# Performance work log

Hardware: AMD Instinct MI355X
Metric: run time of the kernel (lower is better)

Reference implementation:

```python
import jax, jax.numpy as jnp
import numpy as np

N = 50000
E = 800000
D = 128
H = 8
DH = D // H


def setup_inputs() -> dict:
    key = jax.random.key(0)
    ks = jax.random.split(key, 8)
    x = jax.random.normal(ks[0], (N, D), dtype=jnp.float32)
    src = jax.random.randint(ks[1], (E,), 0, N, dtype=jnp.int32)
    dst = jax.random.randint(ks[2], (E,), 0, N, dtype=jnp.int32)
    s = 1.0 / np.sqrt(D)
    w_qkv = jax.random.uniform(ks[3], (3 * D, D), jnp.float32, -s, s)
    b_qkv = jax.random.uniform(ks[4], (3 * D,), jnp.float32, -s, s)
    w_out = jax.random.uniform(ks[5], (D, D), jnp.float32, -s, s)
    b_out = jax.random.uniform(ks[6], (D,), jnp.float32, -s, s)
    return {"x": x, "src": src, "dst": dst, "w_qkv": w_qkv, "b_qkv": b_qkv,
            "w_out": w_out, "b_out": b_out}


def reference(x, src, dst, w_qkv, b_qkv, w_out, b_out):
    n = x.shape[0]
    coef = 1.0 / np.sqrt(DH)
    qkv = (x @ w_qkv.T + b_qkv).reshape(n, H, 3 * DH)
    q, k, v = qkv[..., :DH], qkv[..., DH:2 * DH], qkv[..., 2 * DH:]
    # per-edge scores: dot(k[src], q[dst]) per head -> [E, H]
    scores = jnp.einsum('ehd,ehd->eh', k[src], q[dst]) * coef
    # edge softmax over edges sharing the same destination node
    smax = jax.ops.segment_max(scores, dst, num_segments=n)  # [N, H]
    smax = jnp.where(jnp.isfinite(smax), smax, 0.0)
    ex = jnp.exp(scores - smax[dst])                          # [E, H]
    denom = jax.ops.segment_sum(ex, dst, num_segments=n)      # [N, H]
    probs = ex / jnp.maximum(denom[dst], 1e-30)
    # weighted aggregation of source values -> [N, H, DH]
    agg = jax.ops.segment_sum(probs[:, :, None] * v[src], dst, num_segments=n)
    out = agg.reshape(n, D) @ w_out.T + b_out
    return out
```

## Files before the change

### kernel.cpp

```cpp
#include <hip/hip_runtime.h>
#include <math.h>

#define DD   128
#define NQKV 384
#define CAP  128

typedef __attribute__((ext_vector_type(8))) short          bf16x8;
typedef __attribute__((ext_vector_type(8))) unsigned short ushort8;
typedef __attribute__((ext_vector_type(4))) float          f32x4;
typedef __attribute__((ext_vector_type(2))) float          f32x2;

__device__ __forceinline__ unsigned short f2bf(float f) {
    unsigned u = __float_as_uint(f);
    u += 0x7fffu + ((u >> 16) & 1u);
    return (unsigned short)(u >> 16);
}
__device__ __forceinline__ float bflo(unsigned u) { return __uint_as_float(u << 16); }
__device__ __forceinline__ float bfhi(unsigned u) { return __uint_as_float(u & 0xffff0000u); }

__device__ __forceinline__ unsigned char f2e4m3(float f) {
    float a = f * 0x1p-120f;
    unsigned u = __float_as_uint(a);
    unsigned s = (u >> 24) & 0x80u;
    u &= 0x7fffffffu;
    u += 0x7ffffu + ((u >> 20) & 1u);
    unsigned mag = u >> 20;
    if (mag > 0x7eu) mag = 0x7eu;
    return (unsigned char)(s | mag);
}
__device__ __forceinline__ float e4m3f(unsigned w, int k) {
    unsigned t = w << (24 - 8 * k);
    return __uint_as_float((t & 0x80000000u) | ((t & 0x7f000000u) >> 4));
}

#if defined(__has_builtin) && __has_builtin(__builtin_amdgcn_cvt_pk_f32_fp8)
#define HW_FP8 1
#define DEC4(w, dlo, dhi)                                                   \
    f32x2 dlo = __builtin_amdgcn_cvt_pk_f32_fp8((w), 0);                    \
    f32x2 dhi = __builtin_amdgcn_cvt_pk_f32_fp8((w), 1);
#define QSCALE 1.0f
#else
#define HW_FP8 0
#define DEC4(w, dlo, dhi)                                                   \
    f32x2 dlo, dhi;                                                         \
    dlo.x = e4m3f((w), 0); dlo.y = e4m3f((w), 1);                           \
    dhi.x = e4m3f((w), 2); dhi.y = e4m3f((w), 3);
#define QSCALE 0x1p120f
#endif

#define NWQ8 (NQKV * DD / 8)
#define NWO8 (DD * DD / 8)

__global__ void prep_kernel(const float* __restrict__ x,
                            const float* __restrict__ w_qkv, const float* __restrict__ w_out,
                            unsigned short* __restrict__ xbf,
                            unsigned short* __restrict__ wqb, unsigned short* __restrict__ wob,
                            int* __restrict__ counts, int nzc4, int nx8) {
    int i = blockIdx.x * blockDim.x + threadIdx.x;
    if (i < nzc4) {
        ((int4*)counts)[i] = make_int4(0, 0, 0, 0);
        return;
    }
    int j = i - nzc4;
    const float* s;
    unsigned short* d;
    if (j < NWQ8)              { s = w_qkv + (size_t)j * 8; d = wqb + (size_t)j * 8; }
    else if (j < NWQ8 + NWO8)  { int k = j - NWQ8; s = w_out + (size_t)k * 8; d = wob + (size_t)k * 8; }
    else {
        int k = j - NWQ8 - NWO8;
        if (k >= nx8) return;
        s = x + (size_t)k * 8; d = xbf + (size_t)k * 8;
    }
    const float4* p = (const float4*)s;
    float4 a = p[0], b = p[1];
    float v[8] = {a.x, a.y, a.z, a.w, b.x, b.y, b.z, b.w};
    ushort8 vh;
    #pragma unroll
    for (int t = 0; t < 8; ++t) vh[t] = f2bf(v[t]);
    *(ushort8*)d = vh;
}

#define TM 128
#define TN 128
#define GY_QKV 170
#define GX_OUT 196

__global__ __launch_bounds__(256, 2) void scatter_qkv_kernel(
    const int* __restrict__ src, const int* __restrict__ dst,
    int* __restrict__ counts, unsigned short* __restrict__ lists, int E, int nsb,
    const unsigned short* __restrict__ Xb,
    const unsigned short* __restrict__ B,
    const float* __restrict__ bias, unsigned short* __restrict__ Cq,
    unsigned char* __restrict__ Ck8, unsigned short* __restrict__ Cv,
    int M, int mtiles)
{
    __shared__ unsigned short Bs[TN * DD];

    const int grp = (int)blockIdx.x >> 4;
    const int rr_ = (int)blockIdx.x & 15;
    if (rr_ < 7) {
        const int sblk = grp * 7 + rr_;
        if (sblk >= nsb) return;
        int t = sblk * 256 + (int)threadIdx.x;
        int base = t * 8;
        if (base >= E) return;
        if (base + 8 <= E) {
            int4 d0 = *(const int4*)(dst + base);
            int4 d1 = *(const int4*)(dst + base + 4);
            int4 s0 = *(const int4*)(src + base);
            int4 s1 = *(const int4*)(src + base + 4);
            int dd[8] = {d0.x, d0.y, d0.z, d0.w, d1.x, d1.y, d1.z, d1.w};
            int ss[8] = {s0.x, s0.y, s0.z, s0.w, s1.x, s1.y, s1.z, s1.w};
            int pos[8];
            #pragma unroll
            for (int i = 0; i < 8; ++i) pos[i] = atomicAdd(&counts[dd[i]], 1);
            #pragma unroll
            for (int i = 0; i < 8; ++i)
                if (pos[i] < CAP) lists[(size_t)dd[i] * CAP + pos[i]] = (unsigned short)ss[i];
        } else {
            for (int e = base; e < E; ++e) {
                int d = dst[e];
                int pos = atomicAdd(&counts[d], 1);
                if (pos < CAP) lists[(size_t)d * CAP + pos] = (unsigned short)src[e];
            }
        }
        return;
    }

    const int qb = grp * 9 + (rr_ - 7);
    if (qb >= 3 * GY_QKV) return;
    const int tid  = threadIdx.x;
    const int l    = tid & 63;
    const int wv   = tid >> 6;
    const int quad = l >> 4;
    const int l15  = l & 15;
    const int wm   = (wv & 1) * 64;
    const int wn   = (wv >> 1) * 64;
    const int n0   = (qb % 3) * TN;
    const int mt_start = qb / 3;

    const size_t gbase = (size_t)n0 * DD;
    for (int i = tid; i < TN * 16; i += 256) {
        int col = i >> 4, g = i & 15;
        int gs  = g ^ (col & 15);
        *(ushort8*)&Bs[col * DD + gs * 8] = *(const ushort8*)(B + gbase + (size_t)col * DD + g * 8);
    }
    __syncthreads();

    for (int mt0 = mt_start; mt0 < mtiles; mt0 += GY_QKV) {
        const int m0 = mt0 * TM;

        f32x4 acc[4][4];
        #pragma unroll
        for (int i = 0; i < 4; ++i)
            #pragma unroll
            for (int j = 0; j < 4; ++j) acc[i][j] = (f32x4)0.f;

        bf16x8 af[4][4];
        #pragma unroll
        for (int mt = 0; mt < 4; ++mt) {
            const unsigned short* ar = Xb + (size_t)(m0 + wm + mt * 16 + l15) * DD + quad * 8;
            #pragma unroll
            for (int kq = 0; kq < 4; ++kq) af[mt][kq] = *(const bf16x8*)(ar + kq * 32);
        }

        #pragma unroll
        for (int kq = 0; kq < 4; ++kq) {
            bf16x8 bh[4];
            #pragma unroll
            for (int nt = 0; nt < 4; ++nt) {
                int colL = wn + nt * 16 + l15;
                int gs   = (kq * 4 + quad) ^ (colL & 15);
                bh[nt] = *(const bf16x8*)&Bs[colL * DD + gs * 8];
            }
            #pragma unroll
            for (int mt = 0; mt < 4; ++mt)
                #pragma unroll
                for (int nt = 0; nt < 4; ++nt)
                    acc[mt][nt] = __builtin_amdgcn_mfma_f32_16x16x32_bf16(af[mt][kq], bh[nt], acc[mt][nt], 0, 0, 0);
        }

        #pragma unroll
        for (int nt = 0; nt < 4; ++nt) {
            int j = n0 + wn + nt * 16 + l15;
            float bj = bias[j];
            int h = j / 48;
            int r = j - h * 48;
            int seg = (r >= 32) ? 2 : ((r >= 16) ? 1 : 0);
            int bc  = h * 16 + r - seg * 16;
            if (seg == 1) {
                #pragma unroll
                for (int mt = 0; mt < 4; ++mt)
                    #pragma unroll
                    for (int rr = 0; rr < 4; ++rr) {
                        int m = m0 + wm + mt * 16 + quad * 4 + rr;
                        if (m < M) Ck8[(size_t)m * DD + bc] = f2e4m3(acc[mt][nt][rr] + bj);
                    }
            } else {
                unsigned short* dstp = (seg == 0 ? Cq : Cv);
                #pragma unroll
                for (int mt = 0; mt < 4; ++mt)
                    #pragma unroll
                    for (int rr = 0; rr < 4; ++rr) {
                        int m = m0 + wm + mt * 16 + quad * 4 + rr;
                        if (m < M) dstp[(size_t)m * DD + bc] = f2bf(acc[mt][nt][rr] + bj);
                    }
            }
        }
    }
}

__global__ __launch_bounds__(256, 2) void out_gemm_kernel(
    const unsigned short* __restrict__ A,
    const unsigned short* __restrict__ B,
    const float* __restrict__ bias, float* __restrict__ C, int M, int mtiles)
{
    __shared__ unsigned short Bs[TN * DD];

    const int tid  = threadIdx.x;
    const int l    = tid & 63;
    const int wv   = tid >> 6;
    const int quad = l >> 4;
    const int l15  = l & 15;
    const int wm   = (wv & 1) * 64;
    const int wn   = (wv >> 1) * 64;

    for (int i = tid; i < TN * 16; i += 256) {
        int col = i >> 4, g = i & 15;
        int gs  = g ^ (col & 15);
        *(ushort8*)&Bs[col * DD + gs * 8] = *(const ushort8*)(B + (size_t)col * DD + g * 8);
    }
    __syncthreads();

    for (int mt0 = blockIdx.x; mt0 < mtiles; mt0 += gridDim.x) {
        const int m0 = mt0 * TM;

        f32x4 acc[4][4];
        #pragma unroll
        for (int i = 0; i < 4; ++i)
            #pragma unroll
            for (int j = 0; j < 4; ++j) acc[i][j] = (f32x4)0.f;

        bf16x8 af[4][4];
        #pragma unroll
        for (int mt = 0; mt < 4; ++mt) {
            const int mrow = m0 + wm + mt * 16 + l15;
            const int mclamp = (mrow < M) ? mrow : (M - 1);
            #pragma unroll
            for (int kq = 0; kq < 4; ++kq)
                af[mt][kq] = *(const bf16x8*)(A + (size_t)mclamp * DD + kq * 32 + quad * 8);
        }

        #pragma unroll
        for (int kq = 0; kq < 4; ++kq) {
            bf16x8 bh[4];
            #pragma unroll
            for (int nt = 0; nt < 4; ++nt) {
                int colL = wn + nt * 16 + l15;
                int gs   = (kq * 4 + quad) ^ (colL & 15);
                bh[nt] = *(const bf16x8*)&Bs[colL * DD + gs * 8];
            }
            #pragma unroll
            for (int mt = 0; mt < 4; ++mt)
                #pragma unroll
                for (int nt = 0; nt < 4; ++nt)
                    acc[mt][nt] = __builtin_amdgcn_mfma_f32_16x16x32_bf16(af[mt][kq], bh[nt], acc[mt][nt], 0, 0, 0);
        }

        #pragma unroll
        for (int nt = 0; nt < 4; ++nt) {
            int j = wn + nt * 16 + l15;
            float bj = bias[j];
            #pragma unroll
            for (int mt = 0; mt < 4; ++mt)
                #pragma unroll
                for (int rr = 0; rr < 4; ++rr) {
                    int m = m0 + wm + mt * 16 + quad * 4 + rr;
                    if (m < M) C[(size_t)m * DD + j] = acc[mt][nt][rr] + bj;
                }
        }
    }
}

#define ATTN_BLOCKS 2048

#define ATTN_STEP(cka, cvv, nka, nvv)                                             \
  {                                                                                \
    const int cnt  = min(8, deg - c);                                              \
    const bool more = (c + 8 < deg);                                               \
    const int nn = (int)lists[row0 + min(c + 16 + e, deg - 1)];                    \
    if (more) {                                                                    \
      nka = *(const uint4*)(kb8 + ((((unsigned)nxt) << 7) + hoff));                \
      _Pragma("unroll")                                                            \
      for (int ee = 0; ee < 8; ++ee)                                               \
        nvv[ee] = *(const unsigned*)(vb8 + ((((unsigned)__shfl(nxt, ee)) << 8) + loff4)); \
    }                                                                              \
                        \
    DEC4(cka.x, dax, day)                                                          \
    float sA = dax.x * q0.x;                                                       \
    sA = fmaf(dax.y, q0.y, sA);                                                    \
    sA = fmaf(day.x, q0.z, sA);                                                    \
    sA = fmaf(day.y, q0.w, sA);                                                    \
    DEC4(cka.y, dbx, dby)                                                          \
    float sB = dbx.x * q1.x;                                                       \
    sB = fmaf(dbx.y, q1.y, sB);                                                    \
    sB = fmaf(dby.x, q1.z, sB);                                                    \
    sB = fmaf(dby.y, q1.w, sB);                                                    \
    DEC4(cka.z, dcx, dcy)                                                          \
    float sC = dcx.x * q2.x;                                                       \
    sC = fmaf(dcx.y, q2.y, sC);                                                    \
    sC = fmaf(dcy.x, q2.z, sC);                                                    \
    sC = fmaf(dcy.y, q2.w, sC);                                                    \
    DEC4(cka.w, ddx, ddy)                                                          \
    float sD = ddx.x * q3.x;                                                       \
    sD = fmaf(ddx.y, q3.y, sD);                                                    \
    sD = fmaf(ddy.x, q3.z, sD);                                                    \
    sD = fmaf(ddy.y, q3.w, sD);                                                    \
    const float s_ = (sA + sB) + (sC + sD);                                        \
    const float pp = __expf(s_ * 0.25f);                           \
    const float p_ = (e < cnt) ? pp : 0.f;                                         \
    l_run += p_;                                                                   \
    _Pragma("unroll")                                                              \
    for (int ee = 0; ee < 8; ++ee) {                                               \
      const float pe = __shfl(p_, lbase | ee);          \
      if ((ee & 1) == 0) {                                                         \
        acc0a = fmaf(pe, bflo(cvv[ee]), acc0a);                                    \
        acc1a = fmaf(pe, bfhi(cvv[ee]), acc1a);                                    \
      } else {                                                                     \
        acc0b = fmaf(pe, bflo(cvv[ee]), acc0b);                                    \
        acc1b = fmaf(pe, bfhi(cvv[ee]), acc1b);                                    \
      }                                                                            \
    }                                                                              \
    nxt = nn;                                                                      \
    c += 8;                                                                        \
  }

__global__ __launch_bounds__(256) void wave_attn_kernel(
    const unsigned short* __restrict__ qbf, const unsigned char* __restrict__ k8,
    const unsigned short* __restrict__ vbf, const unsigned short* __restrict__ lists,
    const int* __restrict__ counts,
    unsigned short* __restrict__ agg, int N)
{
    const int lane   = threadIdx.x & 63;
    const int wid    = blockIdx.x * 4 + (threadIdx.x >> 6);
    const int nwaves = gridDim.x * 4;

    const int h = lane >> 3;
    const int e = lane & 7;
    const unsigned hoff  = (unsigned)h << 4;
    const unsigned loff4 = (unsigned)lane << 2;
    const int lbase = lane & 0x38;

    const char* kb8 = (const char*)k8;
    const char* vb8 = (const char*)vbf;
    const char* qb8 = (const char*)qbf;
    char*       ab8 = (char*)agg;

    for (int n = wid; n < N; n += nwaves) {
        const int deg = min(counts[n], CAP);
        const unsigned ooff = (((unsigned)n) << 8) + loff4;
        if (deg == 0) {
            *(unsigned*)(ab8 + ooff) = 0u;
            continue;
        }

        const int row0 = n * CAP;

        const unsigned qoff = (((unsigned)n) << 8) + ((unsigned)h << 5);
        const uint4 qa = *(const uint4*)(qb8 + qoff);
        const uint4 qb = *(const uint4*)(qb8 + qoff + 16);
        const float S = QSCALE;
        const float4 q0 = make_float4(bflo(qa.x)*S, bfhi(qa.x)*S, bflo(qa.y)*S, bfhi(qa.y)*S);
        const float4 q1 = make_float4(bflo(qa.z)*S, bfhi(qa.z)*S, bflo(qa.w)*S, bfhi(qa.w)*S);
        const float4 q2 = make_float4(bflo(qb.x)*S, bfhi(qb.x)*S, bflo(qb.y)*S, bfhi(qb.y)*S);
        const float4 q3 = make_float4(bflo(qb.z)*S, bfhi(qb.z)*S, bflo(qb.w)*S, bfhi(qb.w)*S);

        const int c0s = (int)lists[row0 + min(e, deg - 1)];
        int nxt       = (int)lists[row0 + min(8 + e, deg - 1)];

        uint4 ka0, ka1;
        unsigned vv0[8], vv1[8];
        {
            ka0 = *(const uint4*)(kb8 + ((((unsigned)c0s) << 7) + hoff));
            #pragma unroll
            for (int ee = 0; ee < 8; ++ee)
                vv0[ee] = *(const unsigned*)(vb8 + ((((unsigned)__shfl(c0s, ee)) << 8) + loff4));
        }
        ka1 = ka0;
        #pragma unroll
        for (int ee = 0; ee < 8; ++ee) vv1[ee] = 0u;

        float l_run = 0.f;
        float acc0a = 0.f, acc0b = 0.f, acc1a = 0.f, acc1b = 0.f;

        int c = 0;
        for (;;) {
            ATTN_STEP(ka0, vv0, ka1, vv1);
            if (c >= deg) break;
            ATTN_STEP(ka1, vv1, ka0, vv0);
            if (c >= deg) break;
        }

        l_run += __shfl_xor(l_run, 1);
        l_run += __shfl_xor(l_run, 2);
        l_run += __shfl_xor(l_run, 4);

        const float inv = 1.f / fmaxf(l_run, 1e-30f);
        const float o0 = (acc0a + acc0b) * inv, o1 = (acc1a + acc1b) * inv;
        *(unsigned*)(ab8 + ooff) = (unsigned)f2bf(o0) | ((unsigned)f2bf(o1) << 16);
    }
}

extern "C" void kernel_launch(void* const* d_in, const int* in_sizes, int n_in,
                              void* d_out, int out_size, void* d_ws, size_t ws_size,
                              hipStream_t stream) {
    const float* x     = (const float*)d_in[0];
    const int*   src   = (const int*)  d_in[1];
    const int*   dst   = (const int*)  d_in[2];
    const float* w_qkv = (const float*)d_in[3];
    const float* b_qkv = (const float*)d_in[4];
    const float* w_out = (const float*)d_in[5];
    const float* b_out = (const float*)d_in[6];
    float* out = (float*)d_out;

    const int N = in_sizes[0] / DD;
    const int E = in_sizes[1];

    typedef unsigned short u16;
    char* ws = (char*)d_ws;
    u16* qbf   = (u16*)ws;           ws += (size_t)N * DD * sizeof(u16);
    unsigned char* k8 = (unsigned char*)ws; ws += (size_t)N * DD;
    u16* vbf   = (u16*)ws;           ws += (size_t)N * DD * sizeof(u16);
    u16* aggb  = (u16*)ws;           ws += (size_t)N * DD * sizeof(u16);
    u16* wqb   = (u16*)ws;           ws += (size_t)NQKV * DD * sizeof(u16);
    u16* wob   = (u16*)ws;           ws += (size_t)DD * DD * sizeof(u16);
    int* counts = (int*)ws;          ws += (size_t)((N + 3) / 4 * 4) * sizeof(int);
    u16* lists  = (u16*)ws;          ws += (size_t)N * CAP * sizeof(u16);

    u16* xbf = aggb;

    const int nx8  = N * DD / 8;
    const int nzc4 = (N + 3) / 4;
    const int npb  = (nzc4 + NWQ8 + NWO8 + nx8 + 255) / 256;
    const int nsb  = ((E + 7) / 8 + 255) / 256;
    const int MB   = (N + TM - 1) / TM;
    const int NQB  = 3 * GY_QKV;
    const int ngrp = max((nsb + 6) / 7, (NQB + 8) / 9);

    prep_kernel<<<npb, 256, 0, stream>>>(x, w_qkv, w_out, xbf, wqb, wob,
                                         counts, nzc4, nx8);
    scatter_qkv_kernel<<<ngrp * 16, 256, 0, stream>>>(
        src, dst, counts, lists, E, nsb,
        xbf, wqb, b_qkv, qbf, k8, vbf, N, MB);

    wave_attn_kernel<<<ATTN_BLOCKS, 256, 0, stream>>>(
        qbf, k8, vbf, lists, counts, aggb, N);

    out_gemm_kernel<<<GX_OUT, 256, 0, stream>>>(
        aggb, wob, b_out, out, N, MB);
}
```

Before: 192.9 us.

## Replace fixed-capacity adjacency lists with CSR via count, prefix scan, scatter

```diff
diff --git a/kernel.cpp b/kernel.cpp
--- a/kernel.cpp
+++ b/kernel.cpp
@@ -3,7 +3,6 @@
 
 #define DD   128
 #define NQKV 384
-#define CAP  128
 
 typedef __attribute__((ext_vector_type(8))) short          bf16x8;
 typedef __attribute__((ext_vector_type(8))) unsigned short ushort8;
@@ -34,13 +33,11 @@
 }
 
 #if defined(__has_builtin) && __has_builtin(__builtin_amdgcn_cvt_pk_f32_fp8)
-#define HW_FP8 1
 #define DEC4(w, dlo, dhi)                                                   \
     f32x2 dlo = __builtin_amdgcn_cvt_pk_f32_fp8((w), 0);                    \
     f32x2 dhi = __builtin_amdgcn_cvt_pk_f32_fp8((w), 1);
 #define QSCALE 1.0f
 #else
-#define HW_FP8 0
 #define DEC4(w, dlo, dhi)                                                   \
     f32x2 dlo, dhi;                                                         \
     dlo.x = e4m3f((w), 0); dlo.y = e4m3f((w), 1);                           \
@@ -53,24 +50,32 @@
 
 __global__ void prep_kernel(const float* __restrict__ x,
                             const float* __restrict__ w_qkv, const float* __restrict__ w_out,
+                            const int* __restrict__ dst,
                             unsigned short* __restrict__ xbf,
                             unsigned short* __restrict__ wqb, unsigned short* __restrict__ wob,
-                            int* __restrict__ counts, int nzc4, int nx8) {
-    int i = blockIdx.x * blockDim.x + threadIdx.x;
-    if (i < nzc4) {
-        ((int4*)counts)[i] = make_int4(0, 0, 0, 0);
+                            int* __restrict__ counts, int nx8, int E) {
+    int j = blockIdx.x * blockDim.x + threadIdx.x;
+    if (j >= NWQ8 + NWO8 + nx8) {
+        int k = j - NWQ8 - NWO8 - nx8;
+        int base = k * 8;
+        if (base >= E) return;
+        if (base + 8 <= E) {
+            int4 d0 = *(const int4*)(dst + base);
+            int4 d1 = *(const int4*)(dst + base + 4);
+            atomicAdd(&counts[d0.x], 1); atomicAdd(&counts[d0.y], 1);
+            atomicAdd(&counts[d0.z], 1); atomicAdd(&counts[d0.w], 1);
+            atomicAdd(&counts[d1.x], 1); atomicAdd(&counts[d1.y], 1);
+            atomicAdd(&counts[d1.z], 1); atomicAdd(&counts[d1.w], 1);
+        } else {
+            for (int e = base; e < E; ++e) atomicAdd(&counts[dst[e]], 1);
+        }
         return;
     }
-    int j = i - nzc4;
     const float* s;
     unsigned short* d;
     if (j < NWQ8)              { s = w_qkv + (size_t)j * 8; d = wqb + (size_t)j * 8; }
     else if (j < NWQ8 + NWO8)  { int k = j - NWQ8; s = w_out + (size_t)k * 8; d = wob + (size_t)k * 8; }
-    else {
-        int k = j - NWQ8 - NWO8;
-        if (k >= nx8) return;
-        s = x + (size_t)k * 8; d = xbf + (size_t)k * 8;
-    }
+    else                       { int k = j - NWQ8 - NWO8; s = x + (size_t)k * 8; d = xbf + (size_t)k * 8; }
     const float4* p = (const float4*)s;
     float4 a = p[0], b = p[1];
     float v[8] = {a.x, a.y, a.z, a.w, b.x, b.y, b.z, b.w};
@@ -80,6 +85,38 @@
     *(ushort8*)d = vh;
 }
 
+#define SCAN_PER 49
+__global__ __launch_bounds__(1024) void prefix_kernel(const int* __restrict__ counts,
+                                                      int* __restrict__ offsets,
+                                                      int* __restrict__ cursors, int N) {
+    __shared__ int sc[1024];
+    const int t = threadIdx.x;
+    const int base = t * SCAN_PER;
+    int s = 0;
+    for (int i = 0; i < SCAN_PER; ++i) {
+        int n = base + i;
+        if (n < N) s += counts[n];
+    }
+    sc[t] = s;
+    __syncthreads();
+    for (int d = 1; d < 1024; d <<= 1) {
+        int v = (t >= d) ? sc[t - d] : 0;
+        __syncthreads();
+        sc[t] += v;
+        __syncthreads();
+    }
+    int off = (t == 0) ? 0 : sc[t - 1];
+    for (int i = 0; i < SCAN_PER; ++i) {
+        int n = base + i;
+        if (n < N) {
+            offsets[n] = off;
+            cursors[n] = off;
+            off += counts[n];
+        }
+    }
+    if (t == 1023) offsets[N] = sc[1023];
+}
+
 #define TM 128
 #define TN 128
 #define GY_QKV 170
@@ -87,7 +124,7 @@
 
 __global__ __launch_bounds__(256, 2) void scatter_qkv_kernel(
     const int* __restrict__ src, const int* __restrict__ dst,
-    int* __restrict__ counts, unsigned short* __restrict__ lists, int E, int nsb,
+    int* __restrict__ cursors, unsigned short* __restrict__ lists, int E, int nsb,
     const unsigned short* __restrict__ Xb,
     const unsigned short* __restrict__ B,
     const float* __restrict__ bias, unsigned short* __restrict__ Cq,
@@ -113,15 +150,13 @@
             int ss[8] = {s0.x, s0.y, s0.z, s0.w, s1.x, s1.y, s1.z, s1.w};
             int pos[8];
             #pragma unroll
-            for (int i = 0; i < 8; ++i) pos[i] = atomicAdd(&counts[dd[i]], 1);
-            #pragma unroll
-            for (int i = 0; i < 8; ++i)
-                if (pos[i] < CAP) lists[(size_t)dd[i] * CAP + pos[i]] = (unsigned short)ss[i];
+            for (int i = 0; i < 8; ++i) pos[i] = atomicAdd(&cursors[dd[i]], 1);
+            #pragma unroll
+            for (int i = 0; i < 8; ++i) lists[pos[i]] = (unsigned short)ss[i];
         } else {
             for (int e = base; e < E; ++e) {
-                int d = dst[e];
-                int pos = atomicAdd(&counts[d], 1);
-                if (pos < CAP) lists[(size_t)d * CAP + pos] = (unsigned short)src[e];
+                int pos = atomicAdd(&cursors[dst[e]], 1);
+                lists[pos] = (unsigned short)src[e];
             }
         }
         return;
@@ -338,7 +373,7 @@
 __global__ __launch_bounds__(256) void wave_attn_kernel(
     const unsigned short* __restrict__ qbf, const unsigned char* __restrict__ k8,
     const unsigned short* __restrict__ vbf, const unsigned short* __restrict__ lists,
-    const int* __restrict__ counts,
+    const int* __restrict__ offsets,
     unsigned short* __restrict__ agg, int N)
 {
     const int lane   = threadIdx.x & 63;
@@ -357,14 +392,13 @@
     char*       ab8 = (char*)agg;
 
     for (int n = wid; n < N; n += nwaves) {
-        const int deg = min(counts[n], CAP);
+        const int row0 = offsets[n];
+        const int deg  = offsets[n + 1] - row0;
         const unsigned ooff = (((unsigned)n) << 8) + loff4;
         if (deg == 0) {
             *(unsigned*)(ab8 + ooff) = 0u;
             continue;
         }
-
-        const int row0 = n * CAP;
 
         const unsigned qoff = (((unsigned)n) << 8) + ((unsigned)h << 5);
         const uint4 qa = *(const uint4*)(qb8 + qoff);
@@ -434,27 +468,31 @@
     u16* aggb  = (u16*)ws;           ws += (size_t)N * DD * sizeof(u16);
     u16* wqb   = (u16*)ws;           ws += (size_t)NQKV * DD * sizeof(u16);
     u16* wob   = (u16*)ws;           ws += (size_t)DD * DD * sizeof(u16);
-    int* counts = (int*)ws;          ws += (size_t)((N + 3) / 4 * 4) * sizeof(int);
-    u16* lists  = (u16*)ws;          ws += (size_t)N * CAP * sizeof(u16);
+    int* counts  = (int*)ws;         ws += (size_t)N * sizeof(int);
+    int* offsets = (int*)ws;         ws += (size_t)(N + 1) * sizeof(int);
+    int* cursors = (int*)ws;         ws += (size_t)N * sizeof(int);
+    u16* lists   = (u16*)ws;         ws += (size_t)((E + 3) / 4 * 4) * sizeof(u16);
 
     u16* xbf = aggb;
 
     const int nx8  = N * DD / 8;
-    const int nzc4 = (N + 3) / 4;
-    const int npb  = (nzc4 + NWQ8 + NWO8 + nx8 + 255) / 256;
-    const int nsb  = ((E + 7) / 8 + 255) / 256;
+    const int nh8  = (E + 7) / 8;
+    const int npb  = (NWQ8 + NWO8 + nx8 + nh8 + 255) / 256;
+    const int nsb  = (nh8 + 255) / 256;
     const int MB   = (N + TM - 1) / TM;
     const int NQB  = 3 * GY_QKV;
     const int ngrp = max((nsb + 6) / 7, (NQB + 8) / 9);
 
-    prep_kernel<<<npb, 256, 0, stream>>>(x, w_qkv, w_out, xbf, wqb, wob,
-                                         counts, nzc4, nx8);
+    hipMemsetAsync(counts, 0, (size_t)N * sizeof(int), stream);
+    prep_kernel<<<npb, 256, 0, stream>>>(x, w_qkv, w_out, dst, xbf, wqb, wob,
+                                         counts, nx8, E);
+    prefix_kernel<<<1, 1024, 0, stream>>>(counts, offsets, cursors, N);
     scatter_qkv_kernel<<<ngrp * 16, 256, 0, stream>>>(
-        src, dst, counts, lists, E, nsb,
+        src, dst, cursors, lists, E, nsb,
         xbf, wqb, b_qkv, qbf, k8, vbf, N, MB);
 
     wave_attn_kernel<<<ATTN_BLOCKS, 256, 0, stream>>>(
-        qbf, k8, vbf, lists, counts, aggb, N);
+        qbf, k8, vbf, lists, offsets, aggb, N);
 
     out_gemm_kernel<<<GX_OUT, 256, 0, stream>>>(
         aggb, wob, b_out, out, N, MB);
```

Measured after the change: 355.6 us. +84.4%, slower.

## Fuse output projection into attention kernel via per-wave LDS row and FMA matvec

Applied to the files above, without the earlier changes.

```diff
diff --git a/kernel.cpp b/kernel.cpp
--- a/kernel.cpp
+++ b/kernel.cpp
@@ -34,13 +34,11 @@
 }
 
 #if defined(__has_builtin) && __has_builtin(__builtin_amdgcn_cvt_pk_f32_fp8)
-#define HW_FP8 1
 #define DEC4(w, dlo, dhi)                                                   \
     f32x2 dlo = __builtin_amdgcn_cvt_pk_f32_fp8((w), 0);                    \
     f32x2 dhi = __builtin_amdgcn_cvt_pk_f32_fp8((w), 1);
 #define QSCALE 1.0f
 #else
-#define HW_FP8 0
 #define DEC4(w, dlo, dhi)                                                   \
     f32x2 dlo, dhi;                                                         \
     dlo.x = e4m3f((w), 0); dlo.y = e4m3f((w), 1);                           \
@@ -49,12 +47,11 @@
 #endif
 
 #define NWQ8 (NQKV * DD / 8)
-#define NWO8 (DD * DD / 8)
 
 __global__ void prep_kernel(const float* __restrict__ x,
-                            const float* __restrict__ w_qkv, const float* __restrict__ w_out,
+                            const float* __restrict__ w_qkv,
                             unsigned short* __restrict__ xbf,
-                            unsigned short* __restrict__ wqb, unsigned short* __restrict__ wob,
+                            unsigned short* __restrict__ wqb,
                             int* __restrict__ counts, int nzc4, int nx8) {
     int i = blockIdx.x * blockDim.x + threadIdx.x;
     if (i < nzc4) {
@@ -64,10 +61,9 @@
     int j = i - nzc4;
     const float* s;
     unsigned short* d;
-    if (j < NWQ8)              { s = w_qkv + (size_t)j * 8; d = wqb + (size_t)j * 8; }
-    else if (j < NWQ8 + NWO8)  { int k = j - NWQ8; s = w_out + (size_t)k * 8; d = wob + (size_t)k * 8; }
+    if (j < NWQ8) { s = w_qkv + (size_t)j * 8; d = wqb + (size_t)j * 8; }
     else {
-        int k = j - NWQ8 - NWO8;
+        int k = j - NWQ8;
         if (k >= nx8) return;
         s = x + (size_t)k * 8; d = xbf + (size_t)k * 8;
     }
@@ -83,7 +79,6 @@
 #define TM 128
 #define TN 128
 #define GY_QKV 170
-#define GX_OUT 196
 
 __global__ __launch_bounds__(256, 2) void scatter_qkv_kernel(
     const int* __restrict__ src, const int* __restrict__ dst,
@@ -206,78 +201,6 @@
                         if (m < M) dstp[(size_t)m * DD + bc] = f2bf(acc[mt][nt][rr] + bj);
                     }
             }
-        }
-    }
-}
-
-__global__ __launch_bounds__(256, 2) void out_gemm_kernel(
-    const unsigned short* __restrict__ A,
-    const unsigned short* __restrict__ B,
-    const float* __restrict__ bias, float* __restrict__ C, int M, int mtiles)
-{
-    __shared__ unsigned short Bs[TN * DD];
-
-    const int tid  = threadIdx.x;
-    const int l    = tid & 63;
-    const int wv   = tid >> 6;
-    const int quad = l >> 4;
-    const int l15  = l & 15;
-    const int wm   = (wv & 1) * 64;
-    const int wn   = (wv >> 1) * 64;
-
-    for (int i = tid; i < TN * 16; i += 256) {
-        int col = i >> 4, g = i & 15;
-        int gs  = g ^ (col & 15);
-        *(ushort8*)&Bs[col * DD + gs * 8] = *(const ushort8*)(B + (size_t)col * DD + g * 8);
-    }
-    __syncthreads();
-
-    for (int mt0 = blockIdx.x; mt0 < mtiles; mt0 += gridDim.x) {
-        const int m0 = mt0 * TM;
-
-        f32x4 acc[4][4];
-        #pragma unroll
-        for (int i = 0; i < 4; ++i)
-            #pragma unroll
-            for (int j = 0; j < 4; ++j) acc[i][j] = (f32x4)0.f;
-
-        bf16x8 af[4][4];
-        #pragma unroll
-        for (int mt = 0; mt < 4; ++mt) {
-            const int mrow = m0 + wm + mt * 16 + l15;
-            const int mclamp = (mrow < M) ? mrow : (M - 1);
-            #pragma unroll
-            for (int kq = 0; kq < 4; ++kq)
-                af[mt][kq] = *(const bf16x8*)(A + (size_t)mclamp * DD + kq * 32 + quad * 8);
-        }
-
-        #pragma unroll
-        for (int kq = 0; kq < 4; ++kq) {
-            bf16x8 bh[4];
-            #pragma unroll
-            for (int nt = 0; nt < 4; ++nt) {
-                int colL = wn + nt * 16 + l15;
-                int gs   = (kq * 4 + quad) ^ (colL & 15);
-                bh[nt] = *(const bf16x8*)&Bs[colL * DD + gs * 8];
-            }
-            #pragma unroll
-            for (int mt = 0; mt < 4; ++mt)
-                #pragma unroll
-                for (int nt = 0; nt < 4; ++nt)
-                    acc[mt][nt] = __builtin_amdgcn_mfma_f32_16x16x32_bf16(af[mt][kq], bh[nt], acc[mt][nt], 0, 0, 0);
-        }
-
-        #pragma unroll
-        for (int nt = 0; nt < 4; ++nt) {
-            int j = wn + nt * 16 + l15;
-            float bj = bias[j];
-            #pragma unroll
-            for (int mt = 0; mt < 4; ++mt)
-                #pragma unroll
-                for (int rr = 0; rr < 4; ++rr) {
-                    int m = m0 + wm + mt * 16 + quad * 4 + rr;
-                    if (m < M) C[(size_t)m * DD + j] = acc[mt][nt][rr] + bj;
-                }
         }
     }
 }
@@ -339,10 +262,14 @@
     const unsigned short* __restrict__ qbf, const unsigned char* __restrict__ k8,
     const unsigned short* __restrict__ vbf, const unsigned short* __restrict__ lists,
     const int* __restrict__ counts,
-    unsigned short* __restrict__ agg, int N)
+    const float* __restrict__ Wout, const float* __restrict__ b_out,
+    float* __restrict__ out, int N)
 {
+    __shared__ float aggrow[4][DD];
+
     const int lane   = threadIdx.x & 63;
-    const int wid    = blockIdx.x * 4 + (threadIdx.x >> 6);
+    const int wv_    = threadIdx.x >> 6;
+    const int wid    = blockIdx.x * 4 + wv_;
     const int nwaves = gridDim.x * 4;
 
     const int h = lane >> 3;
@@ -354,60 +281,86 @@
     const char* kb8 = (const char*)k8;
     const char* vb8 = (const char*)vbf;
     const char* qb8 = (const char*)qbf;
-    char*       ab8 = (char*)agg;
+
+    const float* wr0 = Wout + (size_t)(lane * 2) * DD;
+    const float* wr1 = wr0 + DD;
+    const float bo0 = b_out[lane * 2];
+    const float bo1 = b_out[lane * 2 + 1];
 
     for (int n = wid; n < N; n += nwaves) {
         const int deg = min(counts[n], CAP);
-        const unsigned ooff = (((unsigned)n) << 8) + loff4;
-        if (deg == 0) {
-            *(unsigned*)(ab8 + ooff) = 0u;
-            continue;
-        }
-
-        const int row0 = n * CAP;
-
-        const unsigned qoff = (((unsigned)n) << 8) + ((unsigned)h << 5);
-        const uint4 qa = *(const uint4*)(qb8 + qoff);
-        const uint4 qb = *(const uint4*)(qb8 + qoff + 16);
-        const float S = QSCALE;
-        const float4 q0 = make_float4(bflo(qa.x)*S, bfhi(qa.x)*S, bflo(qa.y)*S, bfhi(qa.y)*S);
-        const float4 q1 = make_float4(bflo(qa.z)*S, bfhi(qa.z)*S, bflo(qa.w)*S, bfhi(qa.w)*S);
-        const float4 q2 = make_float4(bflo(qb.x)*S, bfhi(qb.x)*S, bflo(qb.y)*S, bfhi(qb.y)*S);
-        const float4 q3 = make_float4(bflo(qb.z)*S, bfhi(qb.z)*S, bflo(qb.w)*S, bfhi(qb.w)*S);
-
-        const int c0s = (int)lists[row0 + min(e, deg - 1)];
-        int nxt       = (int)lists[row0 + min(8 + e, deg - 1)];
-
-        uint4 ka0, ka1;
-        unsigned vv0[8], vv1[8];
+        float o0 = 0.f, o1 = 0.f;
+
+        if (deg > 0) {
+            const int row0 = n * CAP;
+
+            const unsigned qoff = (((unsigned)n) << 8) + ((unsigned)h << 5);
+            const uint4 qa = *(const uint4*)(qb8 + qoff);
+            const uint4 qb = *(const uint4*)(qb8 + qoff + 16);
+            const float S = QSCALE;
+            const float4 q0 = make_float4(bflo(qa.x)*S, bfhi(qa.x)*S, bflo(qa.y)*S, bfhi(qa.y)*S);
+            const float4 q1 = make_float4(bflo(qa.z)*S, bfhi(qa.z)*S, bflo(qa.w)*S, bfhi(qa.w)*S);
+            const float4 q2 = make_float4(bflo(qb.x)*S, bfhi(qb.x)*S, bflo(qb.y)*S, bfhi(qb.y)*S);
+            const float4 q3 = make_float4(bflo(qb.z)*S, bfhi(qb.z)*S, bflo(qb.w)*S, bfhi(qb.w)*S);
+
+            const int c0s = (int)lists[row0 + min(e, deg - 1)];
+            int nxt       = (int)lists[row0 + min(8 + e, deg - 1)];
+
+            uint4 ka0, ka1;
+            unsigned vv0[8], vv1[8];
+            {
+                ka0 = *(const uint4*)(kb8 + ((((unsigned)c0s) << 7) + hoff));
+                #pragma unroll
+                for (int ee = 0; ee < 8; ++ee)
+                    vv0[ee] = *(const unsigned*)(vb8 + ((((unsigned)__shfl(c0s, ee)) << 8) + loff4));
+            }
+            ka1 = ka0;
+            #pragma unroll
+            for (int ee = 0; ee < 8; ++ee) vv1[ee] = 0u;
+
+            float l_run = 0.f;
+            float acc0a = 0.f, acc0b = 0.f, acc1a = 0.f, acc1b = 0.f;
+
+            int c = 0;
+            for (;;) {
+                ATTN_STEP(ka0, vv0, ka1, vv1);
+                if (c >= deg) break;
+                ATTN_STEP(ka1, vv1, ka0, vv0);
+                if (c >= deg) break;
+            }
+
+            l_run += __shfl_xor(l_run, 1);
+            l_run += __shfl_xor(l_run, 2);
+            l_run += __shfl_xor(l_run, 4);
+
+            const float inv = 1.f / fmaxf(l_run, 1e-30f);
+            o0 = (acc0a + acc0b) * inv;
+            o1 = (acc1a + acc1b) * inv;
+        }
+
+        f32x2 av2;
+        av2.x = bflo((unsigned)f2bf(o0) << 16 >> 16 << 16 ? 0u : 0u);
         {
-            ka0 = *(const uint4*)(kb8 + ((((unsigned)c0s) << 7) + hoff));
-            #pragma unroll
-            for (int ee = 0; ee < 8; ++ee)
-                vv0[ee] = *(const unsigned*)(vb8 + ((((unsigned)__shfl(c0s, ee)) << 8) + loff4));
-        }
-        ka1 = ka0;
-        #pragma unroll
-        for (int ee = 0; ee < 8; ++ee) vv1[ee] = 0u;
-
-        float l_run = 0.f;
-        float acc0a = 0.f, acc0b = 0.f, acc1a = 0.f, acc1b = 0.f;
-
-        int c = 0;
-        for (;;) {
-            ATTN_STEP(ka0, vv0, ka1, vv1);
-            if (c >= deg) break;
-            ATTN_STEP(ka1, vv1, ka0, vv0);
-            if (c >= deg) break;
-        }
-
-        l_run += __shfl_xor(l_run, 1);
-        l_run += __shfl_xor(l_run, 2);
-        l_run += __shfl_xor(l_run, 4);
-
-        const float inv = 1.f / fmaxf(l_run, 1e-30f);
-        const float o0 = (acc0a + acc0b) * inv, o1 = (acc1a + acc1b) * inv;
-        *(unsigned*)(ab8 + ooff) = (unsigned)f2bf(o0) | ((unsigned)f2bf(o1) << 16);
+            float r0 = bflo((unsigned)f2bf(o0));
+            float r1 = bflo((unsigned)f2bf(o1));
+            *(f32x2*)&aggrow[wv_][lane * 2] = (f32x2){r0, r1};
+        }
+
+        float m0 = 0.f, m0b = 0.f, m1 = 0.f, m1b = 0.f;
+        #pragma unroll 4
+        for (int kc = 0; kc < DD; kc += 4) {
+            const float4 av = *(const float4*)&aggrow[wv_][kc];
+            const float4 wa = *(const float4*)(wr0 + kc);
+            const float4 wb = *(const float4*)(wr1 + kc);
+            m0  = fmaf(av.x, wa.x, m0);  m0  = fmaf(av.y, wa.y, m0);
+            m0b = fmaf(av.z, wa.z, m0b); m0b = fmaf(av.w, wa.w, m0b);
+            m1  = fmaf(av.x, wb.x, m1);  m1  = fmaf(av.y, wb.y, m1);
+            m1b = fmaf(av.z, wb.z, m1b); m1b = fmaf(av.w, wb.w, m1b);
+        }
+        f32x2 o;
+        o.x = m0 + m0b + bo0;
+        o.y = m1 + m1b + bo1;
+        *(f32x2*)(out + (size_t)n * DD + lane * 2) = o;
     }
 }
 
@@ -431,31 +384,24 @@
     u16* qbf   = (u16*)ws;           ws += (size_t)N * DD * sizeof(u16);
     unsigned char* k8 = (unsigned char*)ws; ws += (size_t)N * DD;
     u16* vbf   = (u16*)ws;           ws += (size_t)N * DD * sizeof(u16);
-    u16* aggb  = (u16*)ws;           ws += (size_t)N * DD * sizeof(u16);
+    u16* xbf   = (u16*)ws;           ws += (size_t)N * DD * sizeof(u16);
     u16* wqb   = (u16*)ws;           ws += (size_t)NQKV * DD * sizeof(u16);
-    u16* wob   = (u16*)ws;           ws += (size_t)DD * DD * sizeof(u16);
     int* counts = (int*)ws;          ws += (size_t)((N + 3) / 4 * 4) * sizeof(int);
     u16* lists  = (u16*)ws;          ws += (size_t)N * CAP * sizeof(u16);
 
-    u16* xbf = aggb;
-
     const int nx8  = N * DD / 8;
     const int nzc4 = (N + 3) / 4;
-    const int npb  = (nzc4 + NWQ8 + NWO8 + nx8 + 255) / 256;
+    const int npb  = (nzc4 + NWQ8 + nx8 + 255) / 256;
     const int nsb  = ((E + 7) / 8 + 255) / 256;
     const int MB   = (N + TM - 1) / TM;
     const int NQB  = 3 * GY_QKV;
     const int ngrp = max((nsb + 6) / 7, (NQB + 8) / 9);
 
-    prep_kernel<<<npb, 256, 0, stream>>>(x, w_qkv, w_out, xbf, wqb, wob,
-                                         counts, nzc4, nx8);
+    prep_kernel<<<npb, 256, 0, stream>>>(x, w_qkv, xbf, wqb, counts, nzc4, nx8);
     scatter_qkv_kernel<<<ngrp * 16, 256, 0, stream>>>(
         src, dst, counts, lists, E, nsb,
         xbf, wqb, b_qkv, qbf, k8, vbf, N, MB);
 
     wave_attn_kernel<<<ATTN_BLOCKS, 256, 0, stream>>>(
-        qbf, k8, vbf, lists, counts, aggb, N);
-
-    out_gemm_kernel<<<GX_OUT, 256, 0, stream>>>(
-        aggb, wob, b_out, out, N, MB);
-}
+        qbf, k8, vbf, lists, counts, w_out, b_out, out, N);
+}
```

New measurement: 520.3 us. 170% more time.
